# Optimization experiments

Measured on AMD Instinct MI355X. Metric: run time of the kernel, lower is better.

The kernel has to match this reference:

```python
import jax, jax.numpy as jnp
import numpy as np

WS = (8, 8)          # window size
NHEAD = 6
D_MODEL = 192

def _rel_pos_index(ws):
    coords = np.stack(np.meshgrid(np.arange(ws[0]), np.arange(ws[1]), indexing='ij'))  # (2, wh, ww)
    cf = coords.reshape(2, -1)                          # (2, N)
    rel = cf[:, :, None] - cf[:, None, :]               # (2, N, N)
    rel = rel.transpose(1, 2, 0).astype(np.int64)       # (N, N, 2)
    rel[:, :, 0] += ws[0] - 1
    rel[:, :, 1] += ws[1] - 1
    rel[:, :, 0] *= 2 * ws[1] - 1
    return rel.sum(-1)                                  # (N, N)

REL_IDX = jnp.asarray(_rel_pos_index(WS))

def setup_inputs() -> dict:
    key = jax.random.key(0)
    ks = jax.random.split(key, 6)
    B, H, W, C = 4, 256, 256, D_MODEL
    x = jax.random.normal(ks[0], (B, H * W, C), dtype=jnp.float32)
    qkv_w = jax.random.normal(ks[1], (3 * C, C), dtype=jnp.float32) * 0.02
    qkv_b = jnp.zeros((3 * C,), dtype=jnp.float32)
    proj_w = jax.random.normal(ks[2], (C, C), dtype=jnp.float32) * 0.02
    proj_b = jnp.zeros((C,), dtype=jnp.float32)
    n_bias = (2 * WS[0] - 1) * (2 * WS[1] - 1)
    rpb_table = jax.random.normal(ks[3], (n_bias, NHEAD), dtype=jnp.float32) * 0.02
    return {"x": x, "qkv_w": qkv_w, "qkv_b": qkv_b, "proj_w": proj_w,
            "proj_b": proj_b, "rpb_table": rpb_table, "H": H, "W": W}

def reference(x, qkv_w, qkv_b, proj_w, proj_b, rpb_table, H, W):
    B, Ni, C = x.shape
    h, d = NHEAD, C // NHEAD
    wh, ww = WS
    nH, nW = H // wh, W // ww
    N = wh * ww
    # window partition: (B, H, W, C) -> (B*nH*nW, N, C)
    xw = x.reshape(B, nH, wh, nW, ww, C).transpose(0, 1, 3, 2, 4, 5).reshape(-1, N, C)
    qkv = xw @ qkv_w.T + qkv_b                           # (B_, N, 3C)
    B_ = xw.shape[0]
    qkv = qkv.reshape(B_, N, 3, h, d).transpose(2, 0, 3, 1, 4)  # (3, B_, h, N, d)
    q, k, v = qkv[0], qkv[1], qkv[2]
    scale = d ** -0.5
    attn = jnp.einsum('bhnd,bhmd->bhnm', q, k) * scale   # (B_, h, N, N)
    bias = rpb_table[REL_IDX.reshape(-1)].reshape(N, N, h).transpose(2, 0, 1)  # (h, N, N)
    attn = jax.nn.softmax(attn + bias[None], axis=-1)
    out = jnp.einsum('bhnm,bhmd->bhnd', attn, v)         # (B_, h, N, d)
    out = out.transpose(0, 2, 1, 3).reshape(B_, N, C)
    out = out @ proj_w.T + proj_b
    # window reverse: (B*nH*nW, N, C) -> (B, H*W, C)
    out = out.reshape(B, nH, nW, wh, ww, C).transpose(0, 1, 3, 2, 4, 5).reshape(B, Ni, C)
    return out
```

## Files before the change

### kernel.cpp

```cpp
#include <hip/hip_runtime.h>

#define CDIM 192
#define NHEAD 6

typedef __bf16 bf16x8 __attribute__((ext_vector_type(8)));
typedef float f32x4 __attribute__((ext_vector_type(4)));

#define HB     78848
#define Q_OFF  0
#define K_OFF  25600
#define VT_OFF 51200
#define SMEM_BYTES (2 * HB)
#define XS  200
#define QS  200
#define KS  200
#define VTS 72
#define AOS 200
#define PS  72
#define OFS 196
#define SCALE 0.17677669529663687f

__device__ __forceinline__ unsigned short f2b(float f) {
    unsigned int u = __float_as_uint(f);
    u = (u + 0x7FFFu + ((u >> 16) & 1u)) >> 16;
    return (unsigned short)u;
}

#define WS_W1   0
#define WS_W2   221184
#define WS_BIAS 294912

__global__ void prep(const float* __restrict__ qkv_w, const float* __restrict__ proj_w,
                     const float* __restrict__ rpb,
                     unsigned short* __restrict__ W1, unsigned short* __restrict__ W2,
                     float* __restrict__ BIAS) {
    int t = blockIdx.x * 256 + threadIdx.x;
    if (t < 110592) { W1[t] = f2b(qkv_w[t]); return; }
    t -= 110592;
    if (t < 36864)  { W2[t] = f2b(proj_w[t]); return; }
    t -= 36864;
    {
        int h = t >> 12, ij = t & 4095;
        int i = ij >> 6, j = ij & 63;
        int idx = ((i >> 3) - (j >> 3) + 7) * 15 + ((i & 7) - (j & 7) + 7);
        BIAS[t] = rpb[idx * NHEAD + h];
    }
}

__global__ __launch_bounds__(512)
void win_attn(const float* __restrict__ x,
              const unsigned short* __restrict__ qkv_w,
              const float* __restrict__ qkv_b,
              const unsigned short* __restrict__ proj_w,
              const float* __restrict__ proj_b,
              const float* __restrict__ bias,
              float* __restrict__ out)
{
    extern __shared__ __align__(16) char smem[];

    const int tid  = threadIdx.x;
    const int wv   = tid >> 6;
    const int lane = tid & 63;
    const int l15  = lane & 15;
    const int g    = lane >> 4;
    const int g4   = g << 2;
    const int g8   = g << 3;

    long long base[2];
    #pragma unroll
    for (int w = 0; w < 2; ++w) {
        int wid = blockIdx.x * 2 + w;
        int b   = wid >> 10;
        int wy  = (wid >> 5) & 31;
        int wx  = wid & 31;
        base[w] = (long long)(b * 65536 + wy * 8 * 256 + wx * 8) * CDIM;
    }

    #pragma unroll
    for (int w = 0; w < 2; ++w) {
        __bf16* xk = (__bf16*)(smem + w * HB + K_OFF);
        #pragma unroll
        for (int r = 0; r < 6; ++r) {
            int i = tid + r * 512;
            int t = i / 48, part = i - t * 48;
            int iy = t >> 3, ix = t & 7;
            f32x4 v = *(const f32x4*)(x + base[w] + (iy * 256 + ix) * CDIM + part * 4);
            __bf16* dst = xk + t * XS + part * 4;
            dst[0] = (__bf16)v[0]; dst[1] = (__bf16)v[1];
            dst[2] = (__bf16)v[2]; dst[3] = (__bf16)v[3];
        }
    }
    __syncthreads();

    {
        const int qstart_lut[8] = {0, 5, 10, 15, 20, 25, 30, 31};
        const int start = qstart_lut[wv];

        #pragma unroll
        for (int mp = 0; mp < 2; ++mp) {
            f32x4 acc[2][2][5];
            #pragma unroll
            for (int w = 0; w < 2; ++w)
                #pragma unroll
                for (int im = 0; im < 2; ++im)
                    #pragma unroll
                    for (int jn = 0; jn < 5; ++jn)
                        acc[w][im][jn] = (f32x4){0.f, 0.f, 0.f, 0.f};

            #pragma unroll
            for (int kk = 0; kk < 6; ++kk) {
                bf16x8 aa[2][2];
                #pragma unroll
                for (int w = 0; w < 2; ++w) {
                    const __bf16* xk = (const __bf16*)(smem + w * HB + K_OFF);
                    #pragma unroll
                    for (int im = 0; im < 2; ++im)
                        aa[w][im] = *(const bf16x8*)(xk + ((mp * 2 + im) * 16 + l15) * XS + kk * 32 + g8);
                }
                #pragma unroll
                for (int jn = 0; jn < 5; ++jn) {
                    int o = (start + jn) * 16 + l15;
                    bf16x8 bw = *(const bf16x8*)((const __bf16*)qkv_w + o * CDIM + kk * 32 + g8);
                    #pragma unroll
                    for (int w = 0; w < 2; ++w)
                        #pragma unroll
                        for (int im = 0; im < 2; ++im)
                            acc[w][im][jn] = __builtin_amdgcn_mfma_f32_16x16x32_bf16(aa[w][im], bw, acc[w][im][jn], 0, 0, 0);
                }
            }
            __syncthreads();

            #pragma unroll
            for (int jn = 0; jn < 5; ++jn) {
                int nt = start + jn;
                int o  = nt * 16 + l15;
                float qb = qkv_b[o];
                #pragma unroll
                for (int w = 0; w < 2; ++w) {
                    __bf16* ql  = (__bf16*)(smem + w * HB + Q_OFF);
                    __bf16* kl  = (__bf16*)(smem + w * HB + K_OFF);
                    __bf16* vtw = (__bf16*)(smem + w * HB + VT_OFF);
                    #pragma unroll
                    for (int im = 0; im < 2; ++im) {
                        #pragma unroll
                        for (int rr = 0; rr < 4; ++rr) {
                            int tr = (mp * 2 + im) * 16 + g4 + rr;
                            float val = acc[w][im][jn][rr] + qb;
                            if (nt < 12)       ql[tr * QS + o] = (__bf16)val;
                            else if (nt < 24)  kl[tr * KS + (o - 192)] = (__bf16)val;
                            else               vtw[(o - 384) * VTS + tr] = (__bf16)val;
                        }
                    }
                }
            }
        }
    }
    __syncthreads();

    f32x4 sh[3][4];

#define ATTN_A(w) { \
        const __bf16* ql = (const __bf16*)(smem + (w) * HB + Q_OFF); \
        const __bf16* kl = (const __bf16*)(smem + (w) * HB + K_OFF); \
        _Pragma("unroll") \
        for (int u = 0; u < 3; ++u) { \
            int gu = wv * 3 + u; \
            int hu = gu >> 2; \
            int rb = gu & 3; \
            bf16x8 aq = *(const bf16x8*)(ql + (rb * 16 + l15) * QS + hu * 32 + g8); \
            _Pragma("unroll") \
            for (int ni = 0; ni < 4; ++ni) { \
                bf16x8 bk = *(const bf16x8*)(kl + (ni * 16 + l15) * KS + hu * 32 + g8); \
                sh[u][ni] = __builtin_amdgcn_mfma_f32_16x16x32_bf16(aq, bk, (f32x4){0.f, 0.f, 0.f, 0.f}, 0, 0, 0); \
            } \
            const float* brow = bias + hu * 4096; \
            _Pragma("unroll") \
            for (int rr = 0; rr < 4; ++rr) { \
                int row = rb * 16 + g4 + rr; \
                float v0 = sh[u][0][rr] * SCALE + brow[row * 64 +  0 + l15]; \
                float v1 = sh[u][1][rr] * SCALE + brow[row * 64 + 16 + l15]; \
                float v2 = sh[u][2][rr] * SCALE + brow[row * 64 + 32 + l15]; \
                float v3 = sh[u][3][rr] * SCALE + brow[row * 64 + 48 + l15]; \
                float m = fmaxf(fmaxf(v0, v1), fmaxf(v2, v3)); \
                m = fmaxf(m, __shfl_xor(m, 1)); \
                m = fmaxf(m, __shfl_xor(m, 2)); \
                m = fmaxf(m, __shfl_xor(m, 4)); \
                m = fmaxf(m, __shfl_xor(m, 8)); \
                v0 = __expf(v0 - m); v1 = __expf(v1 - m); \
                v2 = __expf(v2 - m); v3 = __expf(v3 - m); \
                float s = v0 + v1 + v2 + v3; \
                s += __shfl_xor(s, 1); s += __shfl_xor(s, 2); \
                s += __shfl_xor(s, 4); s += __shfl_xor(s, 8); \
                float inv = 1.0f / s; \
                sh[u][0][rr] = v0 * inv; \
                sh[u][1][rr] = v1 * inv; \
                sh[u][2][rr] = v2 * inv; \
                sh[u][3][rr] = v3 * inv; \
            } \
        } \
    }

#define ATTN_B(w) { \
        __bf16* ph  = (__bf16*)(smem + (w) * HB + Q_OFF) + wv * (16 * PS); \
        const __bf16* vtw = (const __bf16*)(smem + (w) * HB + VT_OFF); \
        __bf16* aob = (__bf16*)(smem + (w) * HB + K_OFF); \
        _Pragma("unroll") \
        for (int u = 0; u < 3; ++u) { \
            int gu = wv * 3 + u; \
            int hu = gu >> 2; \
            int rb = gu & 3; \
            _Pragma("unroll") \
            for (int rr = 0; rr < 4; ++rr) { \
                int pr = (g4 + rr) * PS; \
                ph[pr +  0 + l15] = (__bf16)sh[u][0][rr]; \
                ph[pr + 16 + l15] = (__bf16)sh[u][1][rr]; \
                ph[pr + 32 + l15] = (__bf16)sh[u][2][rr]; \
                ph[pr + 48 + l15] = (__bf16)sh[u][3][rr]; \
            } \
            __threadfence_block(); \
            f32x4 oacc[2]; \
            oacc[0] = (f32x4){0.f, 0.f, 0.f, 0.f}; \
            oacc[1] = (f32x4){0.f, 0.f, 0.f, 0.f}; \
            _Pragma("unroll") \
            for (int kk = 0; kk < 2; ++kk) { \
                bf16x8 pa = *(const bf16x8*)(ph + l15 * PS + kk * 32 + g8); \
                _Pragma("unroll") \
                for (int nj = 0; nj < 2; ++nj) { \
                    bf16x8 bv = *(const bf16x8*)(vtw + (hu * 32 + nj * 16 + l15) * VTS + kk * 32 + g8); \
                    oacc[nj] = __builtin_amdgcn_mfma_f32_16x16x32_bf16(pa, bv, oacc[nj], 0, 0, 0); \
                } \
            } \
            __threadfence_block(); \
            _Pragma("unroll") \
            for (int nj = 0; nj < 2; ++nj) \
                _Pragma("unroll") \
                for (int rr = 0; rr < 4; ++rr) \
                    aob[(rb * 16 + g4 + rr) * AOS + hu * 32 + nj * 16 + l15] = (__bf16)oacc[nj][rr]; \
        } \
    }

    ATTN_A(0)
    __syncthreads();
    ATTN_B(0)
    ATTN_A(1)
    __syncthreads();
    ATTN_B(1)
    __syncthreads();

    {
        const int pstart_lut[8] = {0, 2, 4, 6, 8, 10, 10, 10};
        const int start = pstart_lut[wv];

        f32x4 pacc[2][4][2];
        #pragma unroll
        for (int w = 0; w < 2; ++w)
            #pragma unroll
            for (int mt = 0; mt < 4; ++mt)
                #pragma unroll
                for (int jn = 0; jn < 2; ++jn)
                    pacc[w][mt][jn] = (f32x4){0.f, 0.f, 0.f, 0.f};

        #pragma unroll
        for (int kk = 0; kk < 6; ++kk) {
            bf16x8 bw[2];
            #pragma unroll
            for (int jn = 0; jn < 2; ++jn) {
                int o = (start + jn) * 16 + l15;
                bw[jn] = *(const bf16x8*)((const __bf16*)proj_w + o * CDIM + kk * 32 + g8);
            }
            #pragma unroll
            for (int w = 0; w < 2; ++w) {
                const __bf16* aob = (const __bf16*)(smem + w * HB + K_OFF);
                bf16x8 aa[4];
                #pragma unroll
                for (int mt = 0; mt < 4; ++mt)
                    aa[mt] = *(const bf16x8*)(aob + (mt * 16 + l15) * AOS + kk * 32 + g8);
                #pragma unroll
                for (int jn = 0; jn < 2; ++jn)
                    #pragma unroll
                    for (int mt = 0; mt < 4; ++mt)
                        pacc[w][mt][jn] = __builtin_amdgcn_mfma_f32_16x16x32_bf16(aa[mt], bw[jn], pacc[w][mt][jn], 0, 0, 0);
            }
        }
        __syncthreads();

        #pragma unroll
        for (int jn = 0; jn < 2; ++jn) {
            int o = (start + jn) * 16 + l15;
            float pb = proj_b[o];
            #pragma unroll
            for (int w = 0; w < 2; ++w) {
                float* stagef = (float*)(smem + w * HB);
                #pragma unroll
                for (int mt = 0; mt < 4; ++mt)
                    #pragma unroll
                    for (int rr = 0; rr < 4; ++rr) {
                        int tr = mt * 16 + g4 + rr;
                        stagef[tr * OFS + o] = pacc[w][mt][jn][rr] + pb;
                    }
            }
        }
    }
    __syncthreads();

    #pragma unroll
    for (int w = 0; w < 2; ++w) {
        const float* stagef = (const float*)(smem + w * HB);
        #pragma unroll
        for (int r = 0; r < 6; ++r) {
            int i = tid + r * 512;
            int t = i / 48, part = i - t * 48;
            int iy = t >> 3, ix = t & 7;
            *(f32x4*)(out + base[w] + (iy * 256 + ix) * CDIM + part * 4) =
                *(const f32x4*)(stagef + t * OFS + part * 4);
        }
    }
#undef ATTN_A
#undef ATTN_B
}

extern "C" void kernel_launch(void* const* d_in, const int* in_sizes, int n_in,
                              void* d_out, int out_size, void* d_ws, size_t ws_size,
                              hipStream_t stream) {
    const float* x      = (const float*)d_in[0];
    const float* qkv_w  = (const float*)d_in[1];
    const float* qkv_b  = (const float*)d_in[2];
    const float* proj_w = (const float*)d_in[3];
    const float* proj_b = (const float*)d_in[4];
    const float* rpb    = (const float*)d_in[5];
    float* outp = (float*)d_out;

    char* ws = (char*)d_ws;
    unsigned short* W1 = (unsigned short*)(ws + WS_W1);
    unsigned short* W2 = (unsigned short*)(ws + WS_W2);
    float* BIAS = (float*)(ws + WS_BIAS);

    hipFuncSetAttribute((const void*)win_attn,
                        hipFuncAttributeMaxDynamicSharedMemorySize, SMEM_BYTES);

    prep<<<672, 256, 0, stream>>>(qkv_w, proj_w, rpb, W1, W2, BIAS);
    win_attn<<<2048, 512, SMEM_BYTES, stream>>>(x, W1, qkv_b, W2, proj_b, BIAS, outp);
}
```

Baseline: 370.0 us.

## Write projection output directly to global, repad LDS strides, relax fences

The projection epilogue now stores fp32 results straight from registers to global memory, removing the LDS staging buffer, its barriers and the coalesced copy-out loop. LDS row strides are padded differently (200→204, 72→76) to change bank-conflict patterns. The x load packs four bf16 values into one vector LDS store, and the block fences in the attention P·V step become a single lgkmcnt wait with a schedule barrier. Direct global stores are scalar and strided across lanes, so write coalescing may get worse. The input conversion also switches to the explicit rounding helper.

```diff
diff --git a/kernel.cpp b/kernel.cpp
--- a/kernel.cpp
+++ b/kernel.cpp
@@ -5,20 +5,22 @@
 
 typedef __bf16 bf16x8 __attribute__((ext_vector_type(8)));
 typedef float f32x4 __attribute__((ext_vector_type(4)));
-
-#define HB     78848
+typedef unsigned short u16x4 __attribute__((ext_vector_type(4)));
+
+#define HB     81408
 #define Q_OFF  0
-#define K_OFF  25600
-#define VT_OFF 51200
+#define K_OFF  26112
+#define VT_OFF 52224
 #define SMEM_BYTES (2 * HB)
-#define XS  200
-#define QS  200
-#define KS  200
-#define VTS 72
-#define AOS 200
-#define PS  72
-#define OFS 196
+#define XS  204
+#define QS  204
+#define KS  204
+#define VTS 76
+#define AOS 204
+#define PS  76
 #define SCALE 0.17677669529663687f
+
+#define LGKM0() { asm volatile("s_waitcnt lgkmcnt(0)" ::: "memory"); __builtin_amdgcn_sched_barrier(0); }
 
 __device__ __forceinline__ unsigned short f2b(float f) {
     unsigned int u = __float_as_uint(f);
@@ -76,6 +78,11 @@
         base[w] = (long long)(b * 65536 + wy * 8 * 256 + wx * 8) * CDIM;
     }
 
+    const int qstart_lut[8] = {0, 5, 10, 15, 20, 25, 30, 31};
+    const int pstart_lut[8] = {0, 2, 4, 6, 8, 10, 10, 10};
+    const int qstart = qstart_lut[wv];
+    const int pstart = pstart_lut[wv];
+
     #pragma unroll
     for (int w = 0; w < 2; ++w) {
         __bf16* xk = (__bf16*)(smem + w * HB + K_OFF);
@@ -85,17 +92,14 @@
             int t = i / 48, part = i - t * 48;
             int iy = t >> 3, ix = t & 7;
             f32x4 v = *(const f32x4*)(x + base[w] + (iy * 256 + ix) * CDIM + part * 4);
-            __bf16* dst = xk + t * XS + part * 4;
-            dst[0] = (__bf16)v[0]; dst[1] = (__bf16)v[1];
-            dst[2] = (__bf16)v[2]; dst[3] = (__bf16)v[3];
+            u16x4 h;
+            h[0] = f2b(v[0]); h[1] = f2b(v[1]); h[2] = f2b(v[2]); h[3] = f2b(v[3]);
+            *(u16x4*)(xk + t * XS + part * 4) = h;
         }
     }
     __syncthreads();
 
     {
-        const int qstart_lut[8] = {0, 5, 10, 15, 20, 25, 30, 31};
-        const int start = qstart_lut[wv];
-
         #pragma unroll
         for (int mp = 0; mp < 2; ++mp) {
             f32x4 acc[2][2][5];
@@ -119,7 +123,7 @@
                 }
                 #pragma unroll
                 for (int jn = 0; jn < 5; ++jn) {
-                    int o = (start + jn) * 16 + l15;
+                    int o = (qstart + jn) * 16 + l15;
                     bf16x8 bw = *(const bf16x8*)((const __bf16*)qkv_w + o * CDIM + kk * 32 + g8);
                     #pragma unroll
                     for (int w = 0; w < 2; ++w)
@@ -132,7 +136,7 @@
 
             #pragma unroll
             for (int jn = 0; jn < 5; ++jn) {
-                int nt = start + jn;
+                int nt = qstart + jn;
                 int o  = nt * 16 + l15;
                 float qb = qkv_b[o];
                 #pragma unroll
@@ -217,7 +221,7 @@
                 ph[pr + 32 + l15] = (__bf16)sh[u][2][rr]; \
                 ph[pr + 48 + l15] = (__bf16)sh[u][3][rr]; \
             } \
-            __threadfence_block(); \
+            LGKM0()    \
             f32x4 oacc[2]; \
             oacc[0] = (f32x4){0.f, 0.f, 0.f, 0.f}; \
             oacc[1] = (f32x4){0.f, 0.f, 0.f, 0.f}; \
@@ -230,7 +234,6 @@
                     oacc[nj] = __builtin_amdgcn_mfma_f32_16x16x32_bf16(pa, bv, oacc[nj], 0, 0, 0); \
                 } \
             } \
-            __threadfence_block(); \
             _Pragma("unroll") \
             for (int nj = 0; nj < 2; ++nj) \
                 _Pragma("unroll") \
@@ -248,9 +251,6 @@
     __syncthreads();
 
     {
-        const int pstart_lut[8] = {0, 2, 4, 6, 8, 10, 10, 10};
-        const int start = pstart_lut[wv];
-
         f32x4 pacc[2][4][2];
         #pragma unroll
         for (int w = 0; w < 2; ++w)
@@ -265,7 +265,7 @@
             bf16x8 bw[2];
             #pragma unroll
             for (int jn = 0; jn < 2; ++jn) {
-                int o = (start + jn) * 16 + l15;
+                int o = (pstart + jn) * 16 + l15;
                 bw[jn] = *(const bf16x8*)((const __bf16*)proj_w + o * CDIM + kk * 32 + g8);
             }
             #pragma unroll
@@ -282,37 +282,22 @@
                         pacc[w][mt][jn] = __builtin_amdgcn_mfma_f32_16x16x32_bf16(aa[mt], bw[jn], pacc[w][mt][jn], 0, 0, 0);
             }
         }
-        __syncthreads();
 
         #pragma unroll
         for (int jn = 0; jn < 2; ++jn) {
-            int o = (start + jn) * 16 + l15;
+            int o = (pstart + jn) * 16 + l15;
             float pb = proj_b[o];
             #pragma unroll
             for (int w = 0; w < 2; ++w) {
-                float* stagef = (float*)(smem + w * HB);
                 #pragma unroll
                 for (int mt = 0; mt < 4; ++mt)
                     #pragma unroll
                     for (int rr = 0; rr < 4; ++rr) {
                         int tr = mt * 16 + g4 + rr;
-                        stagef[tr * OFS + o] = pacc[w][mt][jn][rr] + pb;
+                        int iy = tr >> 3, ix = tr & 7;
+                        out[base[w] + (iy * 256 + ix) * CDIM + o] = pacc[w][mt][jn][rr] + pb;
                     }
             }
-        }
-    }
-    __syncthreads();
-
-    #pragma unroll
-    for (int w = 0; w < 2; ++w) {
-        const float* stagef = (const float*)(smem + w * HB);
-        #pragma unroll
-        for (int r = 0; r < 6; ++r) {
-            int i = tid + r * 512;
-            int t = i / 48, part = i - t * 48;
-            int iy = t >> 3, ix = t & 7;
-            *(f32x4*)(out + base[w] + (iy * 256 + ix) * CDIM + part * 4) =
-                *(const f32x4*)(stagef + t * OFS + part * 4);
         }
     }
 #undef ATTN_A
```

Result: slower. 517.0 us (+39.7%).
